# Performance work log

Hardware: AMD Instinct MI355X
Metric: run time of the kernel (lower is better)

The kernel has to match this reference:

```python
import math
import jax, jax.numpy as jnp
import numpy as np
from jax import lax

T, B, I, H = 384, 128, 128, 1024
G = 4 * H
PI_MIX = 0.75
SIGMA1 = math.exp(-1.0)
SIGMA2 = math.exp(-7.0)
LOG2PI = math.log(2.0 * math.pi)


def setup_inputs() -> dict:
    key = jax.random.key(0)
    ks = jax.random.split(key, 13)
    u = lambda k, shape, lo, hi: jax.random.uniform(k, shape, jnp.float32, lo, hi)
    n = lambda k, shape: jax.random.normal(k, shape, jnp.float32)
    return {
        "x": n(ks[0], (T, B, I)),
        "w_ih_mu": u(ks[1], (G, I), -0.05, 0.05),
        "w_ih_rho": u(ks[2], (G, I), -4.0, -1.0),
        "w_ih_eps": n(ks[3], (G, I)),
        "w_hh_mu": u(ks[4], (G, H), -0.05, 0.05),
        "w_hh_rho": u(ks[5], (G, H), -4.0, -1.0),
        "w_hh_eps": n(ks[6], (G, H)),
        "b_ih_mu": u(ks[7], (G,), -0.05, 0.05),
        "b_ih_rho": u(ks[8], (G,), -4.0, -1.0),
        "b_ih_eps": n(ks[9], (G,)),
        "b_hh_mu": u(ks[10], (G,), -0.05, 0.05),
        "b_hh_rho": u(ks[11], (G,), -4.0, -1.0),
        "b_hh_eps": n(ks[12], (G,)),
    }


def _sample_and_kl(mu, rho, eps):
    # weight reparameterization: w = mu + (softplus(rho)+1e-5)*eps
    sigma = jax.nn.softplus(rho) + 1e-5
    w = mu + sigma * eps
    # KL = log q(w|mu,sigma) - log p(w) under scale-mixture prior
    log_post = jnp.sum(-0.5 * LOG2PI - jnp.log(sigma) - 0.5 * ((w - mu) / sigma) ** 2)
    logn = lambda s: jnp.sum(-0.5 * LOG2PI - np.float32(math.log(s)) - 0.5 * (w / s) ** 2)
    mix1 = logn(SIGMA1) + np.float32(math.log(PI_MIX))
    mix2 = logn(SIGMA2) + np.float32(math.log(1.0 - PI_MIX))
    log_prior = jax.nn.logsumexp(jnp.stack([mix1, mix2]))
    return w, log_post - log_prior


def _lstm(x, w_ih, w_hh, b_ih, b_hh):
    # x: [T, B, I]; precompute input projections for all timesteps
    xg = jnp.einsum("tbi,gi->tbg", x, w_ih) + b_ih + b_hh  # [T, B, 4H]
    h0 = jnp.zeros((x.shape[1], H), x.dtype)
    c0 = jnp.zeros((x.shape[1], H), x.dtype)

    def step(carry, xg_t):
        h, c = carry
        gates = xg_t + h @ w_hh.T  # [B, 4H]
        i, f, g, o = jnp.split(gates, 4, axis=-1)
        c = jax.nn.sigmoid(f) * c + jax.nn.sigmoid(i) * jnp.tanh(g)
        h = jax.nn.sigmoid(o) * jnp.tanh(c)
        return (h, c), h

    (h_n, c_n), ys = lax.scan(step, (h0, c0), xg)
    return ys, h_n, c_n


def reference(x, w_ih_mu, w_ih_rho, w_ih_eps, w_hh_mu, w_hh_rho, w_hh_eps,
              b_ih_mu, b_ih_rho, b_ih_eps, b_hh_mu, b_hh_rho, b_hh_eps):
    w_ih, kl1 = _sample_and_kl(w_ih_mu, w_ih_rho, w_ih_eps)
    w_hh, kl2 = _sample_and_kl(w_hh_mu, w_hh_rho, w_hh_eps)
    b_ih, kl3 = _sample_and_kl(b_ih_mu, b_ih_rho, b_ih_eps)
    b_hh, kl4 = _sample_and_kl(b_hh_mu, b_hh_rho, b_hh_eps)
    kl = kl1 + kl2 + kl3 + kl4
    ys, h_n, c_n = _lstm(x, w_ih, w_hh, b_ih, b_hh)
    # match torch layout: output [T,B,H], h_n/c_n [num_layers*num_dirs, B, H]
    return ys, h_n[None], c_n[None], kl
```

## Files before the change

kernel.cpp:

```cpp
#include <hip/hip_runtime.h>
#include <hip/hip_bf16.h>
#include <math.h>


#define T_STEPS 384
#define HID 1024
#define KTOT 1152
#define KPB 2304

#define WS_WG    0ull
#define WS_XBF   9437184ull
#define WS_BSUM  22020096ull
#define WS_ACC   22036480ull
#define WS_FLAGS 22036544ull
#define WS_HBUF  22037568ull
#define WS_ZERO_LEN 1088ull

#define OUT_HN 50331648ull
#define OUT_CN 50462720ull
#define OUT_KL 50593792ull

typedef __bf16 bf16_t;
typedef bf16_t bf16x8 __attribute__((ext_vector_type(8)));
typedef float f32x4 __attribute__((ext_vector_type(4)));

__device__ __forceinline__ unsigned short f2bf(float f) {
  unsigned int u = __float_as_uint(f);
  u += 0x7fffu + ((u >> 16) & 1u);
  return (unsigned short)(u >> 16);
}
__device__ __forceinline__ bf16x8 ld_bf16x8(const void* p) {
  union { uint4 u; bf16x8 v; } c;
  c.u = *(const uint4*)p;
  return c.v;
}
__device__ __forceinline__ bf16x8 u4bf(uint4 u) {
  union { uint4 u; bf16x8 v; } c;
  c.u = u;
  return c.v;
}
__device__ __forceinline__ float sigm(float x) { return 1.f / (1.f + __expf(-x)); }
__device__ __forceinline__ float tanh_fast(float x) {
  float ax = fabsf(x);
  float e = __expf(-2.f * ax);
  float t = (1.f - e) / (1.f + e);
  return copysignf(t, x);
}

__global__ __launch_bounds__(256) void prep_kernel(
    const float* __restrict__ x,
    const float* __restrict__ wim, const float* __restrict__ wir, const float* __restrict__ wie,
    const float* __restrict__ whm, const float* __restrict__ whr, const float* __restrict__ whe,
    const float* __restrict__ bim, const float* __restrict__ bir, const float* __restrict__ bie,
    const float* __restrict__ bhm, const float* __restrict__ bhr, const float* __restrict__ bhe,
    unsigned short* __restrict__ Wg, unsigned short* __restrict__ xbf,
    float* __restrict__ bsum, double* __restrict__ accd)
{
  const int NHH = 4194304, NIH = 524288, NB = 4096, NX = 6291456;
  const int NTOT = NHH + NIH + NB + NX;
  double a0=0,a1=0,a2=0,a3=0,a4=0,a5=0,a6=0,a7=0;
  int stride = gridDim.x * blockDim.x;
  for (int i = blockIdx.x * blockDim.x + threadIdx.x; i < NTOT; i += stride) {
    if (i < NHH) {
      int g = i >> 10, k = i & 1023;
      float sg = log1pf(expf(whr[i])) + 1e-5f;
      float eps = whe[i];
      float w = fmaf(sg, eps, whm[i]);
      Wg[(size_t)g * KTOT + k] = f2bf(w);
      a2 += (double)(logf(sg) + 0.5f * eps * eps);
      a3 += (double)w * (double)w;
    } else if (i < NHH + NIH) {
      int j = i - NHH;
      int g = j >> 7, k = j & 127;
      float sg = log1pf(expf(wir[j])) + 1e-5f;
      float eps = wie[j];
      float w = fmaf(sg, eps, wim[j]);
      Wg[(size_t)g * KTOT + HID + k] = f2bf(w);
      a0 += (double)(logf(sg) + 0.5f * eps * eps);
      a1 += (double)w * (double)w;
    } else if (i < NHH + NIH + NB) {
      int k = i - NHH - NIH;
      float sg1 = log1pf(expf(bir[k])) + 1e-5f;
      float e1 = bie[k];
      float w1 = fmaf(sg1, e1, bim[k]);
      a4 += (double)(logf(sg1) + 0.5f * e1 * e1);
      a5 += (double)w1 * (double)w1;
      float sg2 = log1pf(expf(bhr[k])) + 1e-5f;
      float e2 = bhe[k];
      float w2 = fmaf(sg2, e2, bhm[k]);
      a6 += (double)(logf(sg2) + 0.5f * e2 * e2);
      a7 += (double)w2 * (double)w2;
      bsum[k] = w1 + w2;
    } else {
      int k = i - NHH - NIH - NB;
      xbf[k] = f2bf(x[k]);
    }
  }
  double v[8] = {a0,a1,a2,a3,a4,a5,a6,a7};
  int lane = threadIdx.x & 63, wave = threadIdx.x >> 6;
  __shared__ double red[4][8];
  #pragma unroll
  for (int q = 0; q < 8; ++q) {
    double t = v[q];
    #pragma unroll
    for (int o = 32; o > 0; o >>= 1) t += __shfl_down(t, o, 64);
    if (lane == 0) red[wave][q] = t;
  }
  __syncthreads();
  if (threadIdx.x == 0) {
    #pragma unroll
    for (int q = 0; q < 8; ++q) {
      double s = red[0][q] + red[1][q] + red[2][q] + red[3][q];
      atomicAdd(&accd[q], s);
    }
  }
}

__global__ __launch_bounds__(256, 1) void lstm_kernel(
    const unsigned short* __restrict__ Wg, const unsigned short* __restrict__ xbf,
    const float* __restrict__ bsum, unsigned short* __restrict__ hbuf,
    unsigned int* __restrict__ flags, const double* __restrict__ accd,
    float* __restrict__ out, int P)
{
  extern __shared__ char smem[];
  unsigned short* Wl = (unsigned short*)smem;
  float* gbuf = (float*)(smem + (size_t)64 * KPB);
  const int tid = threadIdx.x, gid = blockIdx.x;
  const int group = gid >> 6, idx = gid & 63, j0 = idx * 16;

  if (gid == 0 && tid == 0) {
    const double L2PI = 1.8378770664093453;
    const double LN_PI = -0.28768207245178085;
    const double LN_1MPI = -1.3862943611198906;
    const double INV2S1 = 3.694528049465325;
    const double INV2S2 = 601302.1420823884;
    double Ns[4] = {524288.0, 4194304.0, 4096.0, 4096.0};
    double kl = 0.0;
    #pragma unroll
    for (int tq = 0; tq < 4; ++tq) {
      double post_acc = accd[2*tq], w2 = accd[2*tq+1];
      double N = Ns[tq];
      double post = -0.5 * N * L2PI - post_acc;
      double m1 = -0.5 * N * L2PI + N * 1.0 - w2 * INV2S1 + LN_PI;
      double m2 = -0.5 * N * L2PI + N * 7.0 - w2 * INV2S2 + LN_1MPI;
      double mx = fmax(m1, m2), mn = fmin(m1, m2);
      double lse = mx + log1p(exp(mn - mx));
      kl += post - lse;
    }
    out[OUT_KL] = (float)kl;
  }

  {
    int r = tid >> 2, c4 = tid & 3;
    int grow = ((r >> 4) << 10) + j0 + (r & 15);
    const uint4* src = (const uint4*)(Wg + (size_t)grow * KTOT);
    uint4* dst = (uint4*)(smem + (size_t)r * KPB);
    int sw = r & 7;
    #pragma unroll
    for (int j = 0; j < 36; ++j) dst[(c4 + 4 * j) ^ sw] = src[c4 + 4 * j];
  }

  const int lane = tid & 63, wave = tid >> 6;
  const int lq = lane >> 4, ln = lane & 15;
  const int mt = wave >> 1;
  const int nt0 = (wave & 1) * 2, nt1 = nt0 + 1;
  const int arow = mt * 16 + ln;

  const char* WB0b = (const char*)Wl + (size_t)(nt0 * 16 + ln) * KPB;
  const char* WB1b = (const char*)Wl + (size_t)(nt1 * 16 + ln) * KPB;
  const int swb = (ln & 7) << 4;
  const int xo = 16 * lq;

  unsigned short* hgrp = hbuf + (size_t)group * (size_t)P * 32768;
  const unsigned short* xrow = xbf + (size_t)(group * 32 + arow) * 128 + 8 * lq;
  unsigned int* fl = flags + group * 64;
  const int hbase = (lq >> 1) * 512 + arow * 16 + 8 * (lq & 1);

  const int b = tid >> 3, jj0 = (tid & 7) * 2;
  const float2 bi0 = *(const float2*)&bsum[j0 + jj0];
  const float2 bi1 = *(const float2*)&bsum[1024 + j0 + jj0];
  const float2 bi2 = *(const float2*)&bsum[2048 + j0 + jj0];
  const float2 bi3 = *(const float2*)&bsum[3072 + j0 + jj0];
  float c0 = 0.f, c1 = 0.f;

  __syncthreads();

  f32x4 acc0 = {0.f,0.f,0.f,0.f}, acc1 = {0.f,0.f,0.f,0.f};
  #pragma unroll
  for (int kk = 0; kk < 4; ++kk) {
    bf16x8 a  = ld_bf16x8(xrow + 32 * kk);
    bf16x8 b0 = ld_bf16x8(WB0b + 2048 + ((xo + 64 * kk) ^ swb));
    bf16x8 b1 = ld_bf16x8(WB1b + 2048 + ((xo + 64 * kk) ^ swb));
    acc0 = __builtin_amdgcn_mfma_f32_16x16x32_bf16(a, b0, acc0, 0, 0, 0);
    acc1 = __builtin_amdgcn_mfma_f32_16x16x32_bf16(a, b1, acc1, 0, 0, 0);
  }

  for (int t = 0; t < T_STEPS; ++t) {
    if (t > 0) {
      if (((t - 1) & (P - 1)) == 0) {
        __builtin_amdgcn_fence(__ATOMIC_ACQUIRE, "agent");
        __builtin_amdgcn_sched_barrier(0);
      }
      const unsigned short* hr = hgrp + (size_t)((t - 1) & (P - 1)) * 32768 + hbase;
      uint4 areg[32];
      #pragma unroll
      for (int kk = 0; kk < 32; ++kk)
        areg[kk] = *(const uint4*)(hr + kk * 1024);
      __builtin_amdgcn_sched_barrier(0);

      f32x4 acc2 = {0.f,0.f,0.f,0.f}, acc3 = {0.f,0.f,0.f,0.f};
      #pragma unroll
      for (int kk = 0; kk < 32; kk += 2) {
        bf16x8 a0 = u4bf(areg[kk]);
        bf16x8 a1 = u4bf(areg[kk + 1]);
        bf16x8 b00 = ld_bf16x8(WB0b + ((xo + 64 * kk) ^ swb));
        bf16x8 b01 = ld_bf16x8(WB1b + ((xo + 64 * kk) ^ swb));
        bf16x8 b10 = ld_bf16x8(WB0b + ((xo + 64 * (kk + 1)) ^ swb));
        bf16x8 b11 = ld_bf16x8(WB1b + ((xo + 64 * (kk + 1)) ^ swb));
        acc0 = __builtin_amdgcn_mfma_f32_16x16x32_bf16(a0, b00, acc0, 0, 0, 0);
        acc1 = __builtin_amdgcn_mfma_f32_16x16x32_bf16(a0, b01, acc1, 0, 0, 0);
        acc2 = __builtin_amdgcn_mfma_f32_16x16x32_bf16(a1, b10, acc2, 0, 0, 0);
        acc3 = __builtin_amdgcn_mfma_f32_16x16x32_bf16(a1, b11, acc3, 0, 0, 0);
      }
      acc0 += acc2;
      acc1 += acc3;
    }
    #pragma unroll
    for (int r = 0; r < 4; ++r) {
      int m = mt * 16 + lq * 4 + r;
      gbuf[m * 68 + nt0 * 16 + ln] = acc0[r];
      gbuf[m * 68 + nt1 * 16 + ln] = acc1[r];
    }
    __syncthreads();

    float2 gi = *(const float2*)&gbuf[b * 68 + jj0];
    float2 gf = *(const float2*)&gbuf[b * 68 + 16 + jj0];
    float2 gg = *(const float2*)&gbuf[b * 68 + 32 + jj0];
    float2 go = *(const float2*)&gbuf[b * 68 + 48 + jj0];
    float c0n = sigm(gf.x + bi1.x) * c0 + sigm(gi.x + bi0.x) * tanh_fast(gg.x + bi2.x);
    float c1n = sigm(gf.y + bi1.y) * c1 + sigm(gi.y + bi0.y) * tanh_fast(gg.y + bi2.y);
    float h0 = sigm(go.x + bi3.x) * tanh_fast(c0n);
    float h1 = sigm(go.y + bi3.y) * tanh_fast(c1n);
    c0 = c0n; c1 = c1n;
    const bool last_t = (t == T_STEPS - 1);

    if (!last_t) {
      unsigned int* hw32 = (unsigned int*)(hgrp + (size_t)(t & (P - 1)) * 32768);
      unsigned int pk = (unsigned)f2bf(h0) | ((unsigned)f2bf(h1) << 16);
      __hip_atomic_store(&hw32[idx * 256 + tid], pk,
                         __ATOMIC_RELAXED, __HIP_MEMORY_SCOPE_AGENT);
      asm volatile("s_waitcnt vmcnt(0)" ::: "memory");
      __syncthreads();
      if (tid == 0)
        __hip_atomic_store(&fl[idx], (unsigned)(t + 1),
                           __ATOMIC_RELAXED, __HIP_MEMORY_SCOPE_AGENT);
    }

    {
      size_t bg = (size_t)(group * 32 + b);
      float2 hs = {h0, h1};
      *(float2*)&out[(size_t)t * 131072 + bg * 1024 + j0 + jj0] = hs;
      if (last_t) {
        *(float2*)&out[OUT_HN + bg * 1024 + j0 + jj0] = hs;
        float2 cs = {c0n, c1n};
        *(float2*)&out[OUT_CN + bg * 1024 + j0 + jj0] = cs;
      }
    }
    if (!last_t) {
      acc0 = (f32x4){0.f,0.f,0.f,0.f};
      acc1 = (f32x4){0.f,0.f,0.f,0.f};
      const unsigned short* xr = xrow + (size_t)(t + 1) * 16384;
      #pragma unroll
      for (int kk = 0; kk < 4; ++kk) {
        bf16x8 a  = ld_bf16x8(xr + 32 * kk);
        bf16x8 b0 = ld_bf16x8(WB0b + 2048 + ((xo + 64 * kk) ^ swb));
        bf16x8 b1 = ld_bf16x8(WB1b + 2048 + ((xo + 64 * kk) ^ swb));
        acc0 = __builtin_amdgcn_mfma_f32_16x16x32_bf16(a, b0, acc0, 0, 0, 0);
        acc1 = __builtin_amdgcn_mfma_f32_16x16x32_bf16(a, b1, acc1, 0, 0, 0);
      }

      const unsigned tgt = (unsigned)(t + 1);
      unsigned v = __hip_atomic_load(&fl[lane], __ATOMIC_RELAXED,
                                     __HIP_MEMORY_SCOPE_AGENT);
      while (__ballot(v < tgt)) {
        __builtin_amdgcn_s_sleep(1);
        v = __hip_atomic_load(&fl[lane], __ATOMIC_RELAXED,
                              __HIP_MEMORY_SCOPE_AGENT);
      }
      __builtin_amdgcn_sched_barrier(0);
    }
  }
}

extern "C" void kernel_launch(void* const* d_in, const int* in_sizes, int n_in,
                              void* d_out, int out_size, void* d_ws, size_t ws_size,
                              hipStream_t stream) {
  const float* x   = (const float*)d_in[0];
  const float* wim = (const float*)d_in[1];
  const float* wir = (const float*)d_in[2];
  const float* wie = (const float*)d_in[3];
  const float* whm = (const float*)d_in[4];
  const float* whr = (const float*)d_in[5];
  const float* whe = (const float*)d_in[6];
  const float* bim = (const float*)d_in[7];
  const float* bir = (const float*)d_in[8];
  const float* bie = (const float*)d_in[9];
  const float* bhm = (const float*)d_in[10];
  const float* bhr = (const float*)d_in[11];
  const float* bhe = (const float*)d_in[12];
  char* ws = (char*)d_ws;
  unsigned short* Wg    = (unsigned short*)(ws + WS_WG);
  unsigned short* xbf   = (unsigned short*)(ws + WS_XBF);
  float*          bsum  = (float*)(ws + WS_BSUM);
  double*         accd  = (double*)(ws + WS_ACC);
  unsigned int*   flags = (unsigned int*)(ws + WS_FLAGS);
  unsigned short* hbuf  = (unsigned short*)(ws + WS_HBUF);
  float* out = (float*)d_out;

  size_t avail = (ws_size > WS_HBUF) ? ws_size - WS_HBUF : (size_t)0;
  int P = 2;
  while (P < 16 && (size_t)(P * 2) * 4ull * 65536ull <= avail) P *= 2;

  hipMemsetAsync(ws + WS_ACC, 0, WS_ZERO_LEN, stream);
  prep_kernel<<<dim3(1024), dim3(256), 0, stream>>>(
      x, wim, wir, wie, whm, whr, whe, bim, bir, bie, bhm, bhr, bhe,
      Wg, xbf, bsum, accd);

  const int SMEM = 64 * KPB + 32 * 68 * 4;
  hipFuncSetAttribute((const void*)lstm_kernel,
                      hipFuncAttributeMaxDynamicSharedMemorySize, SMEM);
  const unsigned short* Wg_c = Wg; const unsigned short* xbf_c = xbf;
  const float* bsum_c = bsum; const double* acc_c = accd;
  void* args[] = {(void*)&Wg_c, (void*)&xbf_c, (void*)&bsum_c,
                  (void*)&hbuf, (void*)&flags, (void*)&acc_c, (void*)&out,
                  (void*)&P};
  hipError_t e = hipLaunchCooperativeKernel((void*)lstm_kernel, dim3(256), dim3(256),
                                            args, (unsigned)SMEM, stream);
  if (e != hipSuccess) {
    lstm_kernel<<<dim3(256), dim3(256), SMEM, stream>>>(Wg_c, xbf_c, bsum_c,
                                                        hbuf, flags, acc_c, out,
                                                        P);
  }
}
```

Measured before the change: 2.694 ms.

## Keep recurrent weight tiles in registers and poll flags from one wave

Each wave now loads its slice of the recurrent and input weights into registers once (64+8 bf16x8 vectors per lane) instead of staging them in swizzled LDS and re-reading them every timestep. This removes per-step LDS traffic for the B operand. The h loads are split into two halves of 16 to limit register pressure. Flags shrink to 16-bit, and only wave 0 spins on them before a block barrier, which cuts redundant polling traffic. The risk is very high VGPR use, which could cause spills.

```diff
diff --git a/kernel.cpp b/kernel.cpp
--- a/kernel.cpp
+++ b/kernel.cpp
@@ -6,7 +6,6 @@
 #define T_STEPS 384
 #define HID 1024
 #define KTOT 1152
-#define KPB 2304
 
 #define WS_WG    0ull
 #define WS_XBF   9437184ull
@@ -119,12 +118,10 @@
 __global__ __launch_bounds__(256, 1) void lstm_kernel(
     const unsigned short* __restrict__ Wg, const unsigned short* __restrict__ xbf,
     const float* __restrict__ bsum, unsigned short* __restrict__ hbuf,
-    unsigned int* __restrict__ flags, const double* __restrict__ accd,
+    unsigned short* __restrict__ flags, const double* __restrict__ accd,
     float* __restrict__ out, int P)
 {
-  extern __shared__ char smem[];
-  unsigned short* Wl = (unsigned short*)smem;
-  float* gbuf = (float*)(smem + (size_t)64 * KPB);
+  __shared__ float gbuf[32 * 68];
   const int tid = threadIdx.x, gid = blockIdx.x;
   const int group = gid >> 6, idx = gid & 63, j0 = idx * 16;
 
@@ -150,30 +147,29 @@
     out[OUT_KL] = (float)kl;
   }
 
-  {
-    int r = tid >> 2, c4 = tid & 3;
-    int grow = ((r >> 4) << 10) + j0 + (r & 15);
-    const uint4* src = (const uint4*)(Wg + (size_t)grow * KTOT);
-    uint4* dst = (uint4*)(smem + (size_t)r * KPB);
-    int sw = r & 7;
-    #pragma unroll
-    for (int j = 0; j < 36; ++j) dst[(c4 + 4 * j) ^ sw] = src[c4 + 4 * j];
-  }
-
   const int lane = tid & 63, wave = tid >> 6;
   const int lq = lane >> 4, ln = lane & 15;
   const int mt = wave >> 1;
   const int nt0 = (wave & 1) * 2, nt1 = nt0 + 1;
   const int arow = mt * 16 + ln;
 
-  const char* WB0b = (const char*)Wl + (size_t)(nt0 * 16 + ln) * KPB;
-  const char* WB1b = (const char*)Wl + (size_t)(nt1 * 16 + ln) * KPB;
-  const int swb = (ln & 7) << 4;
-  const int xo = 16 * lq;
+  const unsigned short* r0 = Wg + (size_t)(nt0 * 1024 + j0 + ln) * KTOT + 8 * lq;
+  const unsigned short* r1 = Wg + (size_t)(nt1 * 1024 + j0 + ln) * KTOT + 8 * lq;
+  bf16x8 B0[32], B1[32], BX0[4], BX1[4];
+  #pragma unroll
+  for (int kk = 0; kk < 32; ++kk) {
+    B0[kk] = ld_bf16x8(r0 + 32 * kk);
+    B1[kk] = ld_bf16x8(r1 + 32 * kk);
+  }
+  #pragma unroll
+  for (int kk = 0; kk < 4; ++kk) {
+    BX0[kk] = ld_bf16x8(r0 + HID + 32 * kk);
+    BX1[kk] = ld_bf16x8(r1 + HID + 32 * kk);
+  }
 
   unsigned short* hgrp = hbuf + (size_t)group * (size_t)P * 32768;
   const unsigned short* xrow = xbf + (size_t)(group * 32 + arow) * 128 + 8 * lq;
-  unsigned int* fl = flags + group * 64;
+  unsigned short* fl = flags + group * 64;
   const int hbase = (lq >> 1) * 512 + arow * 16 + 8 * (lq & 1);
 
   const int b = tid >> 3, jj0 = (tid & 7) * 2;
@@ -183,16 +179,12 @@
   const float2 bi3 = *(const float2*)&bsum[3072 + j0 + jj0];
   float c0 = 0.f, c1 = 0.f;
 
-  __syncthreads();
-
   f32x4 acc0 = {0.f,0.f,0.f,0.f}, acc1 = {0.f,0.f,0.f,0.f};
   #pragma unroll
   for (int kk = 0; kk < 4; ++kk) {
-    bf16x8 a  = ld_bf16x8(xrow + 32 * kk);
-    bf16x8 b0 = ld_bf16x8(WB0b + 2048 + ((xo + 64 * kk) ^ swb));
-    bf16x8 b1 = ld_bf16x8(WB1b + 2048 + ((xo + 64 * kk) ^ swb));
-    acc0 = __builtin_amdgcn_mfma_f32_16x16x32_bf16(a, b0, acc0, 0, 0, 0);
-    acc1 = __builtin_amdgcn_mfma_f32_16x16x32_bf16(a, b1, acc1, 0, 0, 0);
+    bf16x8 a = ld_bf16x8(xrow + 32 * kk);
+    acc0 = __builtin_amdgcn_mfma_f32_16x16x32_bf16(a, BX0[kk], acc0, 0, 0, 0);
+    acc1 = __builtin_amdgcn_mfma_f32_16x16x32_bf16(a, BX1[kk], acc1, 0, 0, 0);
   }
 
   for (int t = 0; t < T_STEPS; ++t) {
@@ -201,26 +193,34 @@
         __builtin_amdgcn_fence(__ATOMIC_ACQUIRE, "agent");
         __builtin_amdgcn_sched_barrier(0);
       }
-      const unsigned short* hr = hgrp + (size_t)((t - 1) & (P - 1)) * 32768 + hbase;
-      uint4 areg[32];
-      #pragma unroll
-      for (int kk = 0; kk < 32; ++kk)
+      const unsigned short* hr =
+          hgrp + (size_t)((t - 1) & (P - 1)) * 32768 + hbase;
+      f32x4 acc2 = {0.f,0.f,0.f,0.f}, acc3 = {0.f,0.f,0.f,0.f};
+      uint4 areg[16];
+      #pragma unroll
+      for (int kk = 0; kk < 16; ++kk)
         areg[kk] = *(const uint4*)(hr + kk * 1024);
       __builtin_amdgcn_sched_barrier(0);
-
-      f32x4 acc2 = {0.f,0.f,0.f,0.f}, acc3 = {0.f,0.f,0.f,0.f};
-      #pragma unroll
-      for (int kk = 0; kk < 32; kk += 2) {
+      #pragma unroll
+      for (int kk = 0; kk < 16; kk += 2) {
         bf16x8 a0 = u4bf(areg[kk]);
         bf16x8 a1 = u4bf(areg[kk + 1]);
-        bf16x8 b00 = ld_bf16x8(WB0b + ((xo + 64 * kk) ^ swb));
-        bf16x8 b01 = ld_bf16x8(WB1b + ((xo + 64 * kk) ^ swb));
-        bf16x8 b10 = ld_bf16x8(WB0b + ((xo + 64 * (kk + 1)) ^ swb));
-        bf16x8 b11 = ld_bf16x8(WB1b + ((xo + 64 * (kk + 1)) ^ swb));
-        acc0 = __builtin_amdgcn_mfma_f32_16x16x32_bf16(a0, b00, acc0, 0, 0, 0);
-        acc1 = __builtin_amdgcn_mfma_f32_16x16x32_bf16(a0, b01, acc1, 0, 0, 0);
-        acc2 = __builtin_amdgcn_mfma_f32_16x16x32_bf16(a1, b10, acc2, 0, 0, 0);
-        acc3 = __builtin_amdgcn_mfma_f32_16x16x32_bf16(a1, b11, acc3, 0, 0, 0);
+        acc0 = __builtin_amdgcn_mfma_f32_16x16x32_bf16(a0, B0[kk], acc0, 0, 0, 0);
+        acc1 = __builtin_amdgcn_mfma_f32_16x16x32_bf16(a0, B1[kk], acc1, 0, 0, 0);
+        acc2 = __builtin_amdgcn_mfma_f32_16x16x32_bf16(a1, B0[kk+1], acc2, 0, 0, 0);
+        acc3 = __builtin_amdgcn_mfma_f32_16x16x32_bf16(a1, B1[kk+1], acc3, 0, 0, 0);
+      }
+      #pragma unroll
+      for (int kk = 0; kk < 16; ++kk)
+        areg[kk] = *(const uint4*)(hr + (16 + kk) * 1024);
+      #pragma unroll
+      for (int kk = 0; kk < 16; kk += 2) {
+        bf16x8 a0 = u4bf(areg[kk]);
+        bf16x8 a1 = u4bf(areg[kk + 1]);
+        acc0 = __builtin_amdgcn_mfma_f32_16x16x32_bf16(a0, B0[16+kk], acc0, 0, 0, 0);
+        acc1 = __builtin_amdgcn_mfma_f32_16x16x32_bf16(a0, B1[16+kk], acc1, 0, 0, 0);
+        acc2 = __builtin_amdgcn_mfma_f32_16x16x32_bf16(a1, B0[17+kk], acc2, 0, 0, 0);
+        acc3 = __builtin_amdgcn_mfma_f32_16x16x32_bf16(a1, B1[17+kk], acc3, 0, 0, 0);
       }
       acc0 += acc2;
       acc1 += acc3;
@@ -252,7 +252,7 @@
       asm volatile("s_waitcnt vmcnt(0)" ::: "memory");
       __syncthreads();
       if (tid == 0)
-        __hip_atomic_store(&fl[idx], (unsigned)(t + 1),
+        __hip_atomic_store(&fl[idx], (unsigned short)(t + 1),
                            __ATOMIC_RELAXED, __HIP_MEMORY_SCOPE_AGENT);
     }
 
@@ -272,22 +272,22 @@
       const unsigned short* xr = xrow + (size_t)(t + 1) * 16384;
       #pragma unroll
       for (int kk = 0; kk < 4; ++kk) {
-        bf16x8 a  = ld_bf16x8(xr + 32 * kk);
-        bf16x8 b0 = ld_bf16x8(WB0b + 2048 + ((xo + 64 * kk) ^ swb));
-        bf16x8 b1 = ld_bf16x8(WB1b + 2048 + ((xo + 64 * kk) ^ swb));
-        acc0 = __builtin_amdgcn_mfma_f32_16x16x32_bf16(a, b0, acc0, 0, 0, 0);
-        acc1 = __builtin_amdgcn_mfma_f32_16x16x32_bf16(a, b1, acc1, 0, 0, 0);
-      }
-
-      const unsigned tgt = (unsigned)(t + 1);
-      unsigned v = __hip_atomic_load(&fl[lane], __ATOMIC_RELAXED,
-                                     __HIP_MEMORY_SCOPE_AGENT);
-      while (__ballot(v < tgt)) {
-        __builtin_amdgcn_s_sleep(1);
-        v = __hip_atomic_load(&fl[lane], __ATOMIC_RELAXED,
-                              __HIP_MEMORY_SCOPE_AGENT);
-      }
-      __builtin_amdgcn_sched_barrier(0);
+        bf16x8 a = ld_bf16x8(xr + 32 * kk);
+        acc0 = __builtin_amdgcn_mfma_f32_16x16x32_bf16(a, BX0[kk], acc0, 0, 0, 0);
+        acc1 = __builtin_amdgcn_mfma_f32_16x16x32_bf16(a, BX1[kk], acc1, 0, 0, 0);
+      }
+
+      if (wave == 0) {
+        const unsigned short tgt = (unsigned short)(t + 1);
+        unsigned short v = __hip_atomic_load(&fl[lane], __ATOMIC_RELAXED,
+                                             __HIP_MEMORY_SCOPE_AGENT);
+        while (__ballot(v < tgt)) {
+          __builtin_amdgcn_s_sleep(2);
+          v = __hip_atomic_load(&fl[lane], __ATOMIC_RELAXED,
+                                __HIP_MEMORY_SCOPE_AGENT);
+        }
+      }
+      __syncthreads();
     }
   }
 }
@@ -313,7 +313,7 @@
   unsigned short* xbf   = (unsigned short*)(ws + WS_XBF);
   float*          bsum  = (float*)(ws + WS_BSUM);
   double*         accd  = (double*)(ws + WS_ACC);
-  unsigned int*   flags = (unsigned int*)(ws + WS_FLAGS);
+  unsigned short* flags = (unsigned short*)(ws + WS_FLAGS);
   unsigned short* hbuf  = (unsigned short*)(ws + WS_HBUF);
   float* out = (float*)d_out;
 
@@ -326,19 +326,16 @@
       x, wim, wir, wie, whm, whr, whe, bim, bir, bie, bhm, bhr, bhe,
       Wg, xbf, bsum, accd);
 
-  const int SMEM = 64 * KPB + 32 * 68 * 4;
-  hipFuncSetAttribute((const void*)lstm_kernel,
-                      hipFuncAttributeMaxDynamicSharedMemorySize, SMEM);
   const unsigned short* Wg_c = Wg; const unsigned short* xbf_c = xbf;
   const float* bsum_c = bsum; const double* acc_c = accd;
   void* args[] = {(void*)&Wg_c, (void*)&xbf_c, (void*)&bsum_c,
                   (void*)&hbuf, (void*)&flags, (void*)&acc_c, (void*)&out,
                   (void*)&P};
   hipError_t e = hipLaunchCooperativeKernel((void*)lstm_kernel, dim3(256), dim3(256),
-                                            args, (unsigned)SMEM, stream);
+                                            args, 0u, stream);
   if (e != hipSuccess) {
-    lstm_kernel<<<dim3(256), dim3(256), SMEM, stream>>>(Wg_c, xbf_c, bsum_c,
-                                                        hbuf, flags, acc_c, out,
-                                                        P);
-  }
-}
+    lstm_kernel<<<dim3(256), dim3(256), 0, stream>>>(Wg_c, xbf_c, bsum_c,
+                                                     hbuf, flags, acc_c, out,
+                                                     P);
+  }
+}
```

Result: slower. 3.045 ms (+13.0%).

## Use per-wave flags, drop block barrier, pipeline h loads with MFMAs

Applied to the files above, without the earlier changes.

Each wave now publishes its own readiness flag after its h store completes, which removes the block-wide __syncthreads before signalling; consumers poll four flags per producer block. The wave-to-tile mapping changes so each wave owns one N-tile across both batch halves, sharing each B fragment between two MFMAs. The recurrent h loads are staged in chunks of 8 and interleaved with the MFMA chunks to overlap global latency with compute. The x-projection loads are issued before the flag store so they overlap the wait. The cost is more flag traffic and more polling loads per spin iteration.

```diff
diff --git a/kernel.cpp b/kernel.cpp
--- a/kernel.cpp
+++ b/kernel.cpp
@@ -13,8 +13,8 @@
 #define WS_BSUM  22020096ull
 #define WS_ACC   22036480ull
 #define WS_FLAGS 22036544ull
-#define WS_HBUF  22037568ull
-#define WS_ZERO_LEN 1088ull
+#define WS_HBUF  22040640ull
+#define WS_ZERO_LEN 4160ull
 
 #define OUT_HN 50331648ull
 #define OUT_CN 50462720ull
@@ -45,6 +45,36 @@
   float e = __expf(-2.f * ax);
   float t = (1.f - e) / (1.f + e);
   return copysignf(t, x);
+}
+
+__device__ __forceinline__ void stage8(uint4* A0, uint4* A1,
+                                       const unsigned short* hr0,
+                                       const unsigned short* hr1, int c) {
+  #pragma unroll
+  for (int i = 0; i < 8; ++i) {
+    A0[i] = *(const uint4*)(hr0 + (8 * c + i) * 1024);
+    A1[i] = *(const uint4*)(hr1 + (8 * c + i) * 1024);
+  }
+}
+
+__device__ __forceinline__ void mfma8(const uint4* A0, const uint4* A1,
+                                      const char* WBb, int swb, int xo, int c,
+                                      f32x4& a00, f32x4& a01,
+                                      f32x4& a10, f32x4& a11) {
+  #pragma unroll
+  for (int i = 0; i < 8; ++i) {
+    int kk = 8 * c + i;
+    bf16x8 Bf = ld_bf16x8(WBb + ((xo + 64 * kk) ^ swb));
+    bf16x8 a0 = u4bf(A0[i]);
+    bf16x8 a1 = u4bf(A1[i]);
+    if (i & 1) {
+      a01 = __builtin_amdgcn_mfma_f32_16x16x32_bf16(a0, Bf, a01, 0, 0, 0);
+      a11 = __builtin_amdgcn_mfma_f32_16x16x32_bf16(a1, Bf, a11, 0, 0, 0);
+    } else {
+      a00 = __builtin_amdgcn_mfma_f32_16x16x32_bf16(a0, Bf, a00, 0, 0, 0);
+      a10 = __builtin_amdgcn_mfma_f32_16x16x32_bf16(a1, Bf, a10, 0, 0, 0);
+    }
+  }
 }
 
 __global__ __launch_bounds__(256) void prep_kernel(
@@ -162,19 +192,17 @@
 
   const int lane = tid & 63, wave = tid >> 6;
   const int lq = lane >> 4, ln = lane & 15;
-  const int mt = wave >> 1;
-  const int nt0 = (wave & 1) * 2, nt1 = nt0 + 1;
-  const int arow = mt * 16 + ln;
-
-  const char* WB0b = (const char*)Wl + (size_t)(nt0 * 16 + ln) * KPB;
-  const char* WB1b = (const char*)Wl + (size_t)(nt1 * 16 + ln) * KPB;
+
+  const char* WBb = (const char*)Wl + (size_t)(wave * 16 + ln) * KPB;
   const int swb = (ln & 7) << 4;
   const int xo = 16 * lq;
 
   unsigned short* hgrp = hbuf + (size_t)group * (size_t)P * 32768;
-  const unsigned short* xrow = xbf + (size_t)(group * 32 + arow) * 128 + 8 * lq;
-  unsigned int* fl = flags + group * 64;
-  const int hbase = (lq >> 1) * 512 + arow * 16 + 8 * (lq & 1);
+  const unsigned short* xrow0 = xbf + (size_t)(group * 32 + ln) * 128 + 8 * lq;
+  const unsigned short* xrow1 = xrow0 + 16 * 128;
+  unsigned int* flg = flags + group * 256;
+  const int hb0 = (lq >> 1) * 512 + ln * 16 + 8 * (lq & 1);
+  const int hb1 = hb0 + 256;
 
   const int b = tid >> 3, jj0 = (tid & 7) * 2;
   const float2 bi0 = *(const float2*)&bsum[j0 + jj0];
@@ -185,51 +213,47 @@
 
   __syncthreads();
 
-  f32x4 acc0 = {0.f,0.f,0.f,0.f}, acc1 = {0.f,0.f,0.f,0.f};
+  f32x4 accx0 = {0.f,0.f,0.f,0.f}, accx1 = {0.f,0.f,0.f,0.f};
   #pragma unroll
   for (int kk = 0; kk < 4; ++kk) {
-    bf16x8 a  = ld_bf16x8(xrow + 32 * kk);
-    bf16x8 b0 = ld_bf16x8(WB0b + 2048 + ((xo + 64 * kk) ^ swb));
-    bf16x8 b1 = ld_bf16x8(WB1b + 2048 + ((xo + 64 * kk) ^ swb));
-    acc0 = __builtin_amdgcn_mfma_f32_16x16x32_bf16(a, b0, acc0, 0, 0, 0);
-    acc1 = __builtin_amdgcn_mfma_f32_16x16x32_bf16(a, b1, acc1, 0, 0, 0);
+    bf16x8 bx = ld_bf16x8(WBb + 2048 + ((xo + 64 * kk) ^ swb));
+    bf16x8 a0 = ld_bf16x8(xrow0 + 32 * kk);
+    bf16x8 a1 = ld_bf16x8(xrow1 + 32 * kk);
+    accx0 = __builtin_amdgcn_mfma_f32_16x16x32_bf16(a0, bx, accx0, 0, 0, 0);
+    accx1 = __builtin_amdgcn_mfma_f32_16x16x32_bf16(a1, bx, accx1, 0, 0, 0);
   }
 
   for (int t = 0; t < T_STEPS; ++t) {
+    f32x4 acc0, acc1;
     if (t > 0) {
       if (((t - 1) & (P - 1)) == 0) {
         __builtin_amdgcn_fence(__ATOMIC_ACQUIRE, "agent");
         __builtin_amdgcn_sched_barrier(0);
       }
-      const unsigned short* hr = hgrp + (size_t)((t - 1) & (P - 1)) * 32768 + hbase;
-      uint4 areg[32];
-      #pragma unroll
-      for (int kk = 0; kk < 32; ++kk)
-        areg[kk] = *(const uint4*)(hr + kk * 1024);
-      __builtin_amdgcn_sched_barrier(0);
-
-      f32x4 acc2 = {0.f,0.f,0.f,0.f}, acc3 = {0.f,0.f,0.f,0.f};
-      #pragma unroll
-      for (int kk = 0; kk < 32; kk += 2) {
-        bf16x8 a0 = u4bf(areg[kk]);
-        bf16x8 a1 = u4bf(areg[kk + 1]);
-        bf16x8 b00 = ld_bf16x8(WB0b + ((xo + 64 * kk) ^ swb));
-        bf16x8 b01 = ld_bf16x8(WB1b + ((xo + 64 * kk) ^ swb));
-        bf16x8 b10 = ld_bf16x8(WB0b + ((xo + 64 * (kk + 1)) ^ swb));
-        bf16x8 b11 = ld_bf16x8(WB1b + ((xo + 64 * (kk + 1)) ^ swb));
-        acc0 = __builtin_amdgcn_mfma_f32_16x16x32_bf16(a0, b00, acc0, 0, 0, 0);
-        acc1 = __builtin_amdgcn_mfma_f32_16x16x32_bf16(a0, b01, acc1, 0, 0, 0);
-        acc2 = __builtin_amdgcn_mfma_f32_16x16x32_bf16(a1, b10, acc2, 0, 0, 0);
-        acc3 = __builtin_amdgcn_mfma_f32_16x16x32_bf16(a1, b11, acc3, 0, 0, 0);
-      }
-      acc0 += acc2;
-      acc1 += acc3;
+      const unsigned short* hs = hgrp + (size_t)((t - 1) & (P - 1)) * 32768;
+      const unsigned short* hr0 = hs + hb0;
+      const unsigned short* hr1 = hs + hb1;
+      uint4 Aa0[8], Aa1[8], Ab0[8], Ab1[8];
+      f32x4 a00 = accx0, a01 = {0.f,0.f,0.f,0.f};
+      f32x4 a10 = accx1, a11 = {0.f,0.f,0.f,0.f};
+      stage8(Aa0, Aa1, hr0, hr1, 0);  __builtin_amdgcn_sched_barrier(0);
+      stage8(Ab0, Ab1, hr0, hr1, 1);  __builtin_amdgcn_sched_barrier(0);
+      mfma8(Aa0, Aa1, WBb, swb, xo, 0, a00, a01, a10, a11);
+      stage8(Aa0, Aa1, hr0, hr1, 2);  __builtin_amdgcn_sched_barrier(0);
+      mfma8(Ab0, Ab1, WBb, swb, xo, 1, a00, a01, a10, a11);
+      stage8(Ab0, Ab1, hr0, hr1, 3);  __builtin_amdgcn_sched_barrier(0);
+      mfma8(Aa0, Aa1, WBb, swb, xo, 2, a00, a01, a10, a11);
+      mfma8(Ab0, Ab1, WBb, swb, xo, 3, a00, a01, a10, a11);
+      acc0 = a00 + a01;
+      acc1 = a10 + a11;
+    } else {
+      acc0 = accx0;
+      acc1 = accx1;
     }
     #pragma unroll
     for (int r = 0; r < 4; ++r) {
-      int m = mt * 16 + lq * 4 + r;
-      gbuf[m * 68 + nt0 * 16 + ln] = acc0[r];
-      gbuf[m * 68 + nt1 * 16 + ln] = acc1[r];
+      gbuf[(lq * 4 + r) * 68 + wave * 16 + ln] = acc0[r];
+      gbuf[(16 + lq * 4 + r) * 68 + wave * 16 + ln] = acc1[r];
     }
     __syncthreads();
 
@@ -249,13 +273,8 @@
       unsigned int pk = (unsigned)f2bf(h0) | ((unsigned)f2bf(h1) << 16);
       __hip_atomic_store(&hw32[idx * 256 + tid], pk,
                          __ATOMIC_RELAXED, __HIP_MEMORY_SCOPE_AGENT);
-      asm volatile("s_waitcnt vmcnt(0)" ::: "memory");
-      __syncthreads();
-      if (tid == 0)
-        __hip_atomic_store(&fl[idx], (unsigned)(t + 1),
-                           __ATOMIC_RELAXED, __HIP_MEMORY_SCOPE_AGENT);
-    }
-
+      __builtin_amdgcn_sched_barrier(0);
+    }
     {
       size_t bg = (size_t)(group * 32 + b);
       float2 hs = {h0, h1};
@@ -267,25 +286,38 @@
       }
     }
     if (!last_t) {
-      acc0 = (f32x4){0.f,0.f,0.f,0.f};
-      acc1 = (f32x4){0.f,0.f,0.f,0.f};
-      const unsigned short* xr = xrow + (size_t)(t + 1) * 16384;
+      uint4 xa0[4], xa1[4];
+      const unsigned short* xr0 = xrow0 + (size_t)(t + 1) * 16384;
+      const unsigned short* xr1 = xrow1 + (size_t)(t + 1) * 16384;
       #pragma unroll
       for (int kk = 0; kk < 4; ++kk) {
-        bf16x8 a  = ld_bf16x8(xr + 32 * kk);
-        bf16x8 b0 = ld_bf16x8(WB0b + 2048 + ((xo + 64 * kk) ^ swb));
-        bf16x8 b1 = ld_bf16x8(WB1b + 2048 + ((xo + 64 * kk) ^ swb));
-        acc0 = __builtin_amdgcn_mfma_f32_16x16x32_bf16(a, b0, acc0, 0, 0, 0);
-        acc1 = __builtin_amdgcn_mfma_f32_16x16x32_bf16(a, b1, acc1, 0, 0, 0);
+        xa0[kk] = *(const uint4*)(xr0 + 32 * kk);
+        xa1[kk] = *(const uint4*)(xr1 + 32 * kk);
+      }
+      asm volatile("s_waitcnt vmcnt(0)" ::: "memory");
+      __builtin_amdgcn_sched_barrier(0);
+      if (lane == 0)
+        __hip_atomic_store(&flg[idx * 4 + wave], (unsigned)(t + 1),
+                           __ATOMIC_RELAXED, __HIP_MEMORY_SCOPE_AGENT);
+      accx0 = (f32x4){0.f,0.f,0.f,0.f};
+      accx1 = (f32x4){0.f,0.f,0.f,0.f};
+      #pragma unroll
+      for (int kk = 0; kk < 4; ++kk) {
+        bf16x8 bx = ld_bf16x8(WBb + 2048 + ((xo + 64 * kk) ^ swb));
+        accx0 = __builtin_amdgcn_mfma_f32_16x16x32_bf16(u4bf(xa0[kk]), bx, accx0, 0, 0, 0);
+        accx1 = __builtin_amdgcn_mfma_f32_16x16x32_bf16(u4bf(xa1[kk]), bx, accx1, 0, 0, 0);
       }
 
       const unsigned tgt = (unsigned)(t + 1);
-      unsigned v = __hip_atomic_load(&fl[lane], __ATOMIC_RELAXED,
-                                     __HIP_MEMORY_SCOPE_AGENT);
-      while (__ballot(v < tgt)) {
+      const unsigned int* fp = flg + 4 * lane;
+      while (true) {
+        unsigned f0 = __hip_atomic_load(fp + 0, __ATOMIC_RELAXED, __HIP_MEMORY_SCOPE_AGENT);
+        unsigned f1 = __hip_atomic_load(fp + 1, __ATOMIC_RELAXED, __HIP_MEMORY_SCOPE_AGENT);
+        unsigned f2 = __hip_atomic_load(fp + 2, __ATOMIC_RELAXED, __HIP_MEMORY_SCOPE_AGENT);
+        unsigned f3 = __hip_atomic_load(fp + 3, __ATOMIC_RELAXED, __HIP_MEMORY_SCOPE_AGENT);
+        unsigned mn = min(min(f0, f1), min(f2, f3));
+        if (!__ballot(mn < tgt)) break;
         __builtin_amdgcn_s_sleep(1);
-        v = __hip_atomic_load(&fl[lane], __ATOMIC_RELAXED,
-                              __HIP_MEMORY_SCOPE_AGENT);
       }
       __builtin_amdgcn_sched_barrier(0);
     }
```

Result: slower. 3.356 ms (+24.6%).
